# Optimization experiments

Measured on AMD Instinct MI355X. Metric: run time of the kernel, lower is better.

Reference implementation:

```python
import jax, jax.numpy as jnp
import numpy as np

NUM_HEADS = 12


def rotate_every_two(x):
    # interleaved rotation: (x0,x1,x2,x3,...) -> (-x1,x0,-x3,x2,...)
    x1 = x[..., ::2]
    x2 = x[..., 1::2]
    return jnp.stack((-x2, x1), axis=-1).reshape(x.shape)


def rope_cos_sin(seq_len, dim):
    # NOTE: faithfully replicates the source: freqs are concatenated
    # ([freqs, freqs]) even though rotation is interleaved.
    inv_freq = 1.0 / 10000.0 ** (jnp.arange(0, dim, 2, dtype=jnp.float32) / dim)
    t = jnp.arange(seq_len, dtype=jnp.float32)
    freqs = t[:, None] * inv_freq[None, :]          # [S, dim/2]
    emb = jnp.concatenate([freqs, freqs], axis=-1)  # [S, dim]
    return jnp.cos(emb)[None, None], jnp.sin(emb)[None, None]  # [1,1,S,dim]


def setup_inputs() -> dict:
    key = jax.random.key(0)
    kx, k1, k2, k3, k4 = jax.random.split(key, 5)
    B, S, D = 1, 4096, 768
    scale = 1.0 / np.sqrt(D)
    x = jax.random.normal(kx, (B, S, D), dtype=jnp.float32)
    W_qkv = jax.random.normal(k1, (D, 3 * D), dtype=jnp.float32) * scale
    b_qkv = jax.random.normal(k2, (3 * D,), dtype=jnp.float32) * 0.01
    W_out = jax.random.normal(k3, (D, D), dtype=jnp.float32) * scale
    b_out = jax.random.normal(k4, (D,), dtype=jnp.float32) * 0.01
    return {"x": x, "W_qkv": W_qkv, "b_qkv": b_qkv, "W_out": W_out, "b_out": b_out}


def reference(x, W_qkv, b_qkv, W_out, b_out):
    B, S, D = x.shape
    H = NUM_HEADS
    hd = D // H
    qkv = x @ W_qkv + b_qkv                         # [B,S,3D]
    qkv = qkv.reshape(B, S, 3, H, hd).transpose(2, 0, 3, 1, 4)  # [3,B,H,S,hd]
    q, k, v = qkv[0], qkv[1], qkv[2]
    cos, sin = rope_cos_sin(S, hd)
    q = q * cos + rotate_every_two(q) * sin
    k = k * cos + rotate_every_two(k) * sin
    scores = jnp.einsum('bhqd,bhkd->bhqk', q, k) / np.float32(np.sqrt(hd))
    probs = jax.nn.softmax(scores, axis=-1)
    ctx = jnp.einsum('bhqk,bhkd->bhqd', probs, v)   # [B,H,S,hd]
    ctx = ctx.transpose(0, 2, 1, 3).reshape(B, S, D)
    return ctx @ W_out + b_out
```

## Files before the change

### kernel.cpp

```cpp
#include <hip/hip_runtime.h>
#include <hip/hip_bf16.h>
#include <math.h>

#define S_LEN 4096
#define DMODEL 768
#define NH 12
#define HD 64

using f32x4 = __attribute__((ext_vector_type(4))) float;
using s16x8 = __attribute__((ext_vector_type(8))) short;

__device__ inline ushort f2bf(float f) {
  union { float f; uint32_t u; } v; v.f = f;
  uint32_t r = v.u + 0x7fffu + ((v.u >> 16) & 1u);
  return (ushort)(r >> 16);
}
__device__ __forceinline__ float fexp2(float x) {
  float r;
  asm("v_exp_f32 %0, %1" : "=v"(r) : "v"(x));
  return r;
}

__device__ __forceinline__ void gload16(const ushort* g, ushort* l) {
  __builtin_amdgcn_global_load_lds(
      (const __attribute__((address_space(1))) unsigned int*)g,
      (__attribute__((address_space(3))) unsigned int*)l, 16, 0, 0);
}

#define QSCL 0.18033688011112042f
#define L2_1E4_D32 0.4152410118655622f

__device__ void tsplit_dev(const float* __restrict__ W, ushort* __restrict__ Th,
                           int R, int C, int bx, int by,
                           int t, float (*tile)[33]) {
  const int tx = t & 31, ty = t >> 5;
  const int c0 = bx * 32, r0 = by * 32;
#pragma unroll
  for (int i = 0; i < 4; ++i)
    tile[ty + 8 * i][tx] = W[(size_t)(r0 + ty + 8 * i) * C + c0 + tx];
  __syncthreads();
#pragma unroll
  for (int i = 0; i < 4; ++i) {
    const float v = tile[tx][ty + 8 * i];
    const size_t off = (size_t)(c0 + ty + 8 * i) * R + r0 + tx;
    Th[off] = f2bf(v);
  }
}

__global__ __launch_bounds__(256) void k_prep(
    const float* __restrict__ x, const float* __restrict__ Wqkv,
    const float* __restrict__ Wout, float* __restrict__ ct,
    float* __restrict__ st, ushort* __restrict__ Wth,
    ushort* __restrict__ Woth, ushort* __restrict__ xh) {
  __shared__ float tile[32][33];
  const int b = blockIdx.x, t = threadIdx.x;
  if (b < 1024) {
    const int s = (b << 2) | (t >> 6), d = t & 63, j = d & 31;
    const float invf = fexp2(-L2_1E4_D32 * (float)j);
    const float af = (float)s * invf;
    ct[s * HD + d] = cosf(af);
    st[s * HD + d] = sinf(af);
  } else if (b < 2752) {
    const int bb = b - 1024;
    tsplit_dev(Wqkv, Wth, DMODEL, 3 * DMODEL, bb % 72, bb / 72, t, tile);
  } else if (b < 3328) {
    const int bb = b - 2752;
    tsplit_dev(Wout, Woth, DMODEL, DMODEL, bb % 24, bb / 24, t, tile);
  } else {
    const int i = (b - 3328) * 256 + t;
    const float4 v = ((const float4*)x)[i];
    ushort4 h;
    h.x = f2bf(v.x); h.y = f2bf(v.y); h.z = f2bf(v.z); h.w = f2bf(v.w);
    ((ushort4*)xh)[i] = h;
  }
}

template <int EPI, int BM, int TERMS>
__global__ __launch_bounds__(256) void k_gemm_split(
    const ushort* __restrict__ Ah, const ushort* __restrict__ Al,
    const ushort* __restrict__ Bh,
    const float* __restrict__ bias,
    const float* __restrict__ ct, const float* __restrict__ st,
    ushort* __restrict__ qh,
    ushort* __restrict__ kh, ushort* __restrict__ vt,
    float* __restrict__ out) {
  constexpr int MF = BM / 32;
  __shared__ __align__(16) ushort SS[(TERMS == 2 ? 2 : 1) * BM * 64 + 8192];
  constexpr int BOFF = (TERMS == 2 ? 2 : 1) * BM * 64;

  const int t = threadIdx.x;
  const int w = t >> 6, l = t & 63, g = l >> 4, lq = l & 15;
  const int wm = w >> 1, wn = w & 1;
  const int nbx = gridDim.x;
  int lin = blockIdx.y * nbx + blockIdx.x;
  const int cpx = (nbx * gridDim.y) >> 3;
  lin = (lin & 7) * cpx + (lin >> 3);
  const int m0 = (lin / nbx) * BM, n0 = (lin % nbx) * 128;

  f32x4 acc[MF][4];
#pragma unroll
  for (int i = 0; i < MF; ++i)
#pragma unroll
    for (int j = 0; j < 4; ++j) acc[i][j] = (f32x4){0.f, 0.f, 0.f, 0.f};

  const ushort* gsrc;
  ushort* lbase;
  int ninst;
  if (TERMS == 2) {
    if (w == 0)      { gsrc = Ah + (size_t)m0 * 768; lbase = SS;               ninst = BM / 16; }
    else if (w == 1) { gsrc = Ah + (size_t)(m0 + BM / 2) * 768; lbase = SS + BM * 32; ninst = BM / 16; }
    else if (w == 2) { gsrc = Al + (size_t)m0 * 768; lbase = SS + BM * 64;     ninst = BM / 8; }
    else             { gsrc = Bh + (size_t)n0 * 768; lbase = SS + BOFF;        ninst = 16; }
  } else {
    if (w == 0)      { gsrc = Ah + (size_t)m0 * 768; lbase = SS;               ninst = BM / 16; }
    else if (w == 1) { gsrc = Ah + (size_t)(m0 + BM / 2) * 768; lbase = SS + BM * 32; ninst = BM / 16; }
    else if (w == 2) { gsrc = Bh + (size_t)n0 * 768; lbase = SS + BOFF;        ninst = 8; }
    else             { gsrc = Bh + (size_t)(n0 + 64) * 768; lbase = SS + BOFF + 4096; ninst = 8; }
  }
  const int grow = l >> 3, gch = l & 7;
  gsrc += (size_t)grow * 768 + ((gch ^ grow) << 3);

  const ushort* rdA[2], * rdB[2];
#pragma unroll
  for (int kk = 0; kk < 2; ++kk) {
    rdA[kk] = SS + wm * (BM / 2) * 64 + lq * 64 + ((((kk << 2) | g) ^ (lq & 7)) << 3);
    rdB[kk] = SS + BOFF + wn * 4096 + lq * 64 + ((((kk << 2) | g) ^ (lq & 7)) << 3);
  }

  for (int kt = 0; kt < 768 / 64; ++kt) {
    __syncthreads();
#pragma unroll
    for (int i = 0; i < 16; ++i)
      if (i < ninst) gload16(gsrc + (size_t)i * (8 * 768) + kt * 64, lbase + i * 512);
    __syncthreads();
#pragma unroll
    for (int kk = 0; kk < 2; ++kk) {
      s16x8 ah[MF], al4[MF];
#pragma unroll
      for (int mf = 0; mf < MF; ++mf) {
        ah[mf] = *(const s16x8*)(rdA[kk] + mf * 1024);
        if (TERMS == 2) al4[mf] = *(const s16x8*)(rdA[kk] + mf * 1024 + BM * 64);
      }
      __builtin_amdgcn_s_setprio(1);
#pragma unroll
      for (int nf = 0; nf < 4; ++nf) {
        const s16x8 bhf = *(const s16x8*)(rdB[kk] + nf * 1024);
#pragma unroll
        for (int mf = 0; mf < MF; ++mf) {
          acc[mf][nf] = __builtin_amdgcn_mfma_f32_16x16x32_bf16(ah[mf], bhf, acc[mf][nf], 0, 0, 0);
          if (TERMS == 2)
            acc[mf][nf] = __builtin_amdgcn_mfma_f32_16x16x32_bf16(al4[mf], bhf, acc[mf][nf], 0, 0, 0);
        }
      }
      __builtin_amdgcn_s_setprio(0);
    }
  }

  if constexpr (EPI == 0) {
    const int cidx = n0 / DMODEL;
    if (cidx < 2) {
      ushort* dh = (cidx == 0) ? qh : kh;
      const float scl = (cidx == 0) ? QSCL : 1.0f;
#pragma unroll
      for (int nf = 0; nf < 4; ++nf) {
        const int n = n0 + wn * 64 + nf * 16 + lq;
        const int rem = n - cidx * DMODEL;
        const int hh = rem >> 6, d = rem & 63;
        const float sgn = (d & 1) ? 1.f : -1.f;
        const float bb = bias[n];
#pragma unroll
        for (int mf = 0; mf < MF; ++mf)
#pragma unroll
          for (int rg = 0; rg < 4; ++rg) {
            const int s = m0 + wm * (BM / 2) + mf * 16 + g * 4 + rg;
            const float v = acc[mf][nf][rg] + bb;
            const float vp = __shfl_xor(v, 1, 64);
            const float o = (v * ct[s * HD + d] + sgn * vp * st[s * HD + d]) * scl;
            const size_t off = (((size_t)hh * S_LEN + s) << 6) + d;
            dh[off] = f2bf(o);
          }
      }
    } else {
#pragma unroll
      for (int nf = 0; nf < 4; ++nf) {
        const int n = n0 + wn * 64 + nf * 16 + lq;
        const int rem = n - 2 * DMODEL;
        const int hh = rem >> 6, d = rem & 63;
        const float bb = bias[n];
#pragma unroll
        for (int mf = 0; mf < MF; ++mf) {
          union { ushort us[4]; ushort4 u4; } u;
#pragma unroll
          for (int rg = 0; rg < 4; ++rg) u.us[rg] = f2bf(acc[mf][nf][rg] + bb);
          const int sb = m0 + wm * (BM / 2) + mf * 16 + g * 4;
          const int sbp = (sb & ~31) | (g << 3) | ((mf & 1) << 2);
          *(ushort4*)(vt + ((size_t)hh * 64 + d) * S_LEN + sbp) = u.u4;
        }
      }
    }
  } else {
#pragma unroll
    for (int nf = 0; nf < 4; ++nf) {
      const int n = n0 + wn * 64 + nf * 16 + lq;
      const float bb = bias[n];
#pragma unroll
      for (int mf = 0; mf < MF; ++mf)
#pragma unroll
        for (int rg = 0; rg < 4; ++rg) {
          const int s = m0 + wm * (BM / 2) + mf * 16 + g * 4 + rg;
          out[(size_t)s * DMODEL + n] = acc[mf][nf][rg] + bb;
        }
    }
  }
}

__global__ __launch_bounds__(256) void k_attn_mfma(
    const ushort* __restrict__ qh,
    const ushort* __restrict__ kh, const ushort* __restrict__ vtp,
    ushort* __restrict__ cxh) {
  const int h = blockIdx.y;
  const int s0 = blockIdx.x << 6;
  const int t = threadIdx.x;
  const int w = t >> 6, l = t & 63, lq = l & 15, g = l >> 4;

  __shared__ __align__(16) ushort Ks0[2 * 4096];
  __shared__ __align__(16) ushort Vs0[2 * 4096];

  s16x8 qa0, qa1;
  {
    const size_t qoff = ((size_t)h * S_LEN + s0 + (w << 4) + lq) * 64 + (g << 3);
    qa0 = *(const s16x8*)(qh + qoff);
    qa1 = *(const s16x8*)(qh + qoff + 32);
  }
  s16x8 ones;
#pragma unroll
  for (int i = 0; i < 8; ++i) ones[i] = (short)0x3F80;

  f32x4 o[4];
#pragma unroll
  for (int m = 0; m < 4; ++m) o[m] = (f32x4){0.f, 0.f, 0.f, 0.f};
  f32x4 lacc = {0.f, 0.f, 0.f, 0.f};

  const int srow0 = (w << 4) + (l >> 3);
  const int sx = ((l & 7) ^ (l >> 3)) << 3;
  const ushort* gk = kh + ((size_t)h * S_LEN + srow0) * 64 + sx;
  const ushort* gv = vtp + (((size_t)h << 6) + srow0) * S_LEN + sx;
  ushort* ldK = Ks0 + srow0 * 64 + ((l & 7) << 3);
  ushort* ldV = Vs0 + srow0 * 64 + ((l & 7) << 3);

  auto stage = [&](const int kt, const int B) {
    const ushort* pk = gk + ((size_t)kt << 12);
    const ushort* pv = gv + (kt << 6);
    gload16(pk, ldK + B * 4096);
    gload16(pk + 512, ldK + B * 4096 + 512);
    gload16(pv, ldV + B * 4096);
    gload16(pv + (size_t)8 * S_LEN, ldV + B * 4096 + 512);
  };

  const int b0 = (lq << 6) | ((g ^ (lq & 7)) << 3);
  const int b1 = (lq << 6) | (((g + 4) ^ (lq & 7)) << 3);
  const ushort* kr0 = Ks0 + b0;
  const ushort* kr1 = Ks0 + b1;
  const ushort* vr0 = Vs0 + b0;
  const ushort* vr1 = Vs0 + b1;

  stage(0, 0);
  __syncthreads();

  auto body = [&](const int kt, const int CUR, const int NX, bool pref) {
    if (pref) stage(kt + 1, NX);

    f32x4 sc[4];
    __builtin_amdgcn_s_setprio(1);
#pragma unroll
    for (int n = 0; n < 4; ++n) {
      const s16x8 ka0 = *(const s16x8*)(kr0 + CUR * 4096 + (n << 10));
      const s16x8 ka1 = *(const s16x8*)(kr1 + CUR * 4096 + (n << 10));
      f32x4 a = {0.f, 0.f, 0.f, 0.f};
      a = __builtin_amdgcn_mfma_f32_16x16x32_bf16(ka0, qa0, a, 0, 0, 0);
      a = __builtin_amdgcn_mfma_f32_16x16x32_bf16(ka1, qa1, a, 0, 0, 0);
      sc[n] = a;
    }
    __builtin_amdgcn_s_setprio(0);

    float pr[4][4];
#pragma unroll
    for (int n = 0; n < 4; ++n)
#pragma unroll
      for (int rg = 0; rg < 4; ++rg) pr[n][rg] = fexp2(sc[n][rg]);

    uint32_t u[8];
#pragma unroll
    for (int n = 0; n < 4; ++n) {
      asm("v_cvt_pk_bf16_f32 %0, %1, %2"
          : "=v"(u[2 * n]) : "v"(pr[n][0]), "v"(pr[n][1]));
      asm("v_cvt_pk_bf16_f32 %0, %1, %2"
          : "=v"(u[2 * n + 1]) : "v"(pr[n][2]), "v"(pr[n][3]));
    }
    union { uint32_t uw[4]; s16x8 v; } p0, p1;
    p0.uw[0] = u[0]; p0.uw[1] = u[1]; p0.uw[2] = u[2]; p0.uw[3] = u[3];
    p1.uw[0] = u[4]; p1.uw[1] = u[5]; p1.uw[2] = u[6]; p1.uw[3] = u[7];

    __builtin_amdgcn_s_setprio(1);
    lacc = __builtin_amdgcn_mfma_f32_16x16x32_bf16(ones, p0.v, lacc, 0, 0, 0);
    lacc = __builtin_amdgcn_mfma_f32_16x16x32_bf16(ones, p1.v, lacc, 0, 0, 0);
#pragma unroll
    for (int m = 0; m < 4; ++m) {
      const s16x8 va0 = *(const s16x8*)(vr0 + CUR * 4096 + (m << 10));
      const s16x8 va1 = *(const s16x8*)(vr1 + CUR * 4096 + (m << 10));
      o[m] = __builtin_amdgcn_mfma_f32_16x16x32_bf16(va0, p0.v, o[m], 0, 0, 0);
      o[m] = __builtin_amdgcn_mfma_f32_16x16x32_bf16(va1, p1.v, o[m], 0, 0, 0);
    }
    __builtin_amdgcn_s_setprio(0);

    __syncthreads();
  };

  for (int p = 0; p < 32; ++p) {
    body(2 * p, 0, 1, true);
    body(2 * p + 1, 1, 0, p < 31);
  }

  const float inv = 1.0f / lacc[0];
  const size_t rowoff = (size_t)(s0 + (w << 4) + lq) * DMODEL + (h << 6) + (g << 2);
  ushort* hrow = cxh + rowoff;
#pragma unroll
  for (int m = 0; m < 4; ++m) {
    const float v0 = o[m][0] * inv, v1 = o[m][1] * inv;
    const float v2 = o[m][2] * inv, v3 = o[m][3] * inv;
    uint32_t h01, h23;
    asm("v_cvt_pk_bf16_f32 %0, %1, %2" : "=v"(h01) : "v"(v0), "v"(v1));
    asm("v_cvt_pk_bf16_f32 %0, %1, %2" : "=v"(h23) : "v"(v2), "v"(v3));
    uint2 hq;
    hq.x = h01; hq.y = h23;
    *(uint2*)(hrow + (m << 4)) = hq;
  }
}

extern "C" void kernel_launch(void* const* d_in, const int* in_sizes, int n_in,
                              void* d_out, int out_size, void* d_ws, size_t ws_size,
                              hipStream_t stream) {
  const float* x    = (const float*)d_in[0];
  const float* Wqkv = (const float*)d_in[1];
  const float* bqkv = (const float*)d_in[2];
  const float* Wout = (const float*)d_in[3];
  const float* bout = (const float*)d_in[4];
  float* out = (float*)d_out;

  const size_t NQ = (size_t)NH * S_LEN * HD;
  const size_t ND = (size_t)S_LEN * DMODEL;
  char* base = (char*)d_ws;
  ushort* qh = (ushort*)base;
  ushort* kh = qh + NQ;
  ushort* vt = kh + NQ;
  ushort* xh = vt + NQ;
  float* ct = (float*)(xh + ND);
  float* st = ct + (size_t)S_LEN * HD;
  ushort* Wth = (ushort*)(st + (size_t)S_LEN * HD);
  ushort* Woth = Wth + (size_t)3 * DMODEL * DMODEL;

  k_prep<<<dim3(6400), dim3(256), 0, stream>>>(
      x, Wqkv, Wout, ct, st, Wth, Woth, xh);
  k_gemm_split<0, 64, 1><<<dim3(3 * DMODEL / 128, S_LEN / 64), dim3(256), 0, stream>>>(
      xh, nullptr, Wth, bqkv, ct, st, qh, kh, vt, nullptr);
  k_attn_mfma<<<dim3(S_LEN / 64, NH), dim3(256), 0, stream>>>(
      qh, kh, vt, xh);
  k_gemm_split<1, 64, 1><<<dim3(DMODEL / 128, S_LEN / 64), dim3(256), 0, stream>>>(
      xh, nullptr, Woth, bout, nullptr, nullptr,
      nullptr, nullptr, nullptr, out);
}
```

Before: 123.2 us.

## Triple-buffer K/V tiles in attention with prefetch distance two

The attention kernel's K/V shared-memory staging grows from two buffers to three, so tile p+2 is loaded while tile p is computed. The per-iteration __syncthreads is replaced by an explicit s_waitcnt vmcnt(4) plus s_barrier, letting the newest prefetch stay in flight across the barrier. The aim is to hide more global-load latency behind the MFMA work. In exchange, LDS per block grows to 48KB, which may lower occupancy, and correctness now depends on the hand-written waitcnt counts.

Result: no change. 122.1 us (-0.9%).

```diff
diff --git a/kernel.cpp b/kernel.cpp
--- a/kernel.cpp
+++ b/kernel.cpp
@@ -223,8 +223,8 @@
   const int t = threadIdx.x;
   const int w = t >> 6, l = t & 63, lq = l & 15, g = l >> 4;
 
-  __shared__ __align__(16) ushort Ks0[2 * 4096];
-  __shared__ __align__(16) ushort Vs0[2 * 4096];
+  __shared__ __align__(16) ushort Ks0[3 * 4096];
+  __shared__ __align__(16) ushort Vs0[3 * 4096];
 
   s16x8 qa0, qa1;
   {
@@ -265,17 +265,21 @@
   const ushort* vr1 = Vs0 + b1;
 
   stage(0, 0);
-  __syncthreads();
-
-  auto body = [&](const int kt, const int CUR, const int NX, bool pref) {
-    if (pref) stage(kt + 1, NX);
+  stage(1, 1);
+  asm volatile("s_waitcnt vmcnt(4)" ::: "memory");
+  __builtin_amdgcn_sched_barrier(0);
+  __builtin_amdgcn_s_barrier();
+  __builtin_amdgcn_sched_barrier(0);
+
+  auto body = [&](const int p, const int B, const int NB, const bool pref) {
+    if (pref) stage(p + 2, NB);
 
     f32x4 sc[4];
     __builtin_amdgcn_s_setprio(1);
 #pragma unroll
     for (int n = 0; n < 4; ++n) {
-      const s16x8 ka0 = *(const s16x8*)(kr0 + CUR * 4096 + (n << 10));
-      const s16x8 ka1 = *(const s16x8*)(kr1 + CUR * 4096 + (n << 10));
+      const s16x8 ka0 = *(const s16x8*)(kr0 + B * 4096 + (n << 10));
+      const s16x8 ka1 = *(const s16x8*)(kr1 + B * 4096 + (n << 10));
       f32x4 a = {0.f, 0.f, 0.f, 0.f};
       a = __builtin_amdgcn_mfma_f32_16x16x32_bf16(ka0, qa0, a, 0, 0, 0);
       a = __builtin_amdgcn_mfma_f32_16x16x32_bf16(ka1, qa1, a, 0, 0, 0);
@@ -306,20 +310,27 @@
     lacc = __builtin_amdgcn_mfma_f32_16x16x32_bf16(ones, p1.v, lacc, 0, 0, 0);
 #pragma unroll
     for (int m = 0; m < 4; ++m) {
-      const s16x8 va0 = *(const s16x8*)(vr0 + CUR * 4096 + (m << 10));
-      const s16x8 va1 = *(const s16x8*)(vr1 + CUR * 4096 + (m << 10));
+      const s16x8 va0 = *(const s16x8*)(vr0 + B * 4096 + (m << 10));
+      const s16x8 va1 = *(const s16x8*)(vr1 + B * 4096 + (m << 10));
       o[m] = __builtin_amdgcn_mfma_f32_16x16x32_bf16(va0, p0.v, o[m], 0, 0, 0);
       o[m] = __builtin_amdgcn_mfma_f32_16x16x32_bf16(va1, p1.v, o[m], 0, 0, 0);
     }
     __builtin_amdgcn_s_setprio(0);
 
-    __syncthreads();
+    __builtin_amdgcn_sched_barrier(0);
+    if (pref) asm volatile("s_waitcnt vmcnt(4) lgkmcnt(0)" ::: "memory");
+    else      asm volatile("s_waitcnt vmcnt(0) lgkmcnt(0)" ::: "memory");
+    __builtin_amdgcn_sched_barrier(0);
+    __builtin_amdgcn_s_barrier();
+    __builtin_amdgcn_sched_barrier(0);
   };
 
-  for (int p = 0; p < 32; ++p) {
-    body(2 * p, 0, 1, true);
-    body(2 * p + 1, 1, 0, p < 31);
-  }
+  for (int c = 0; c < 21; ++c) {
+    body(3 * c + 0, 0, 2, true);
+    body(3 * c + 1, 1, 0, true);
+    body(3 * c + 2, 2, 1, c < 20);
+  }
+  body(63, 0, 2, false);
 
   const float inv = 1.0f / lacc[0];
   const size_t rowoff = (size_t)(s0 + (w << 4) + lq) * DMODEL + (h << 6) + (g << 2);
```

## Double-buffer LDS tiles in split GEMM to overlap global loads with MFMA

Applied to the files above, without the earlier changes.

Restructures the GEMM main loop to use two LDS buffers: the next k-tile is issued via global_load_lds into the alternate buffer while MFMAs consume the current one, with a single barrier per iteration. This aims to hide global-load latency and halve barrier count. It also drops the unused two-term (hi/lo) path. LDS usage doubles, which may lower occupancy.

After: 118.1 us. -4.1%, faster.

```diff
diff --git a/kernel.cpp b/kernel.cpp
--- a/kernel.cpp
+++ b/kernel.cpp
@@ -75,18 +75,17 @@
   }
 }
 
-template <int EPI, int BM, int TERMS>
+template <int EPI, int BM>
 __global__ __launch_bounds__(256) void k_gemm_split(
-    const ushort* __restrict__ Ah, const ushort* __restrict__ Al,
-    const ushort* __restrict__ Bh,
+    const ushort* __restrict__ Ah, const ushort* __restrict__ Bh,
     const float* __restrict__ bias,
     const float* __restrict__ ct, const float* __restrict__ st,
     ushort* __restrict__ qh,
     ushort* __restrict__ kh, ushort* __restrict__ vt,
     float* __restrict__ out) {
   constexpr int MF = BM / 32;
-  __shared__ __align__(16) ushort SS[(TERMS == 2 ? 2 : 1) * BM * 64 + 8192];
-  constexpr int BOFF = (TERMS == 2 ? 2 : 1) * BM * 64;
+  constexpr int SSH = BM * 64 + 8192;
+  __shared__ __align__(16) ushort SS[2 * SSH];
 
   const int t = threadIdx.x;
   const int w = t >> 6, l = t & 63, g = l >> 4, lq = l & 15;
@@ -106,54 +105,53 @@
   const ushort* gsrc;
   ushort* lbase;
   int ninst;
-  if (TERMS == 2) {
-    if (w == 0)      { gsrc = Ah + (size_t)m0 * 768; lbase = SS;               ninst = BM / 16; }
-    else if (w == 1) { gsrc = Ah + (size_t)(m0 + BM / 2) * 768; lbase = SS + BM * 32; ninst = BM / 16; }
-    else if (w == 2) { gsrc = Al + (size_t)m0 * 768; lbase = SS + BM * 64;     ninst = BM / 8; }
-    else             { gsrc = Bh + (size_t)n0 * 768; lbase = SS + BOFF;        ninst = 16; }
-  } else {
-    if (w == 0)      { gsrc = Ah + (size_t)m0 * 768; lbase = SS;               ninst = BM / 16; }
-    else if (w == 1) { gsrc = Ah + (size_t)(m0 + BM / 2) * 768; lbase = SS + BM * 32; ninst = BM / 16; }
-    else if (w == 2) { gsrc = Bh + (size_t)n0 * 768; lbase = SS + BOFF;        ninst = 8; }
-    else             { gsrc = Bh + (size_t)(n0 + 64) * 768; lbase = SS + BOFF + 4096; ninst = 8; }
-  }
+  if (w == 0)      { gsrc = Ah + (size_t)m0 * 768;            lbase = SS;                ninst = BM / 16; }
+  else if (w == 1) { gsrc = Ah + (size_t)(m0 + BM / 2) * 768; lbase = SS + BM * 32;      ninst = BM / 16; }
+  else if (w == 2) { gsrc = Bh + (size_t)n0 * 768;            lbase = SS + BM * 64;      ninst = 8; }
+  else             { gsrc = Bh + (size_t)(n0 + 64) * 768;     lbase = SS + BM * 64 + 4096; ninst = 8; }
   const int grow = l >> 3, gch = l & 7;
   gsrc += (size_t)grow * 768 + ((gch ^ grow) << 3);
 
+  auto gstage = [&](const int kt, const int B) {
+#pragma unroll
+    for (int i = 0; i < 16; ++i)
+      if (i < ninst)
+        gload16(gsrc + (size_t)i * (8 * 768) + kt * 64, lbase + B * SSH + i * 512);
+  };
+
   const ushort* rdA[2], * rdB[2];
 #pragma unroll
   for (int kk = 0; kk < 2; ++kk) {
     rdA[kk] = SS + wm * (BM / 2) * 64 + lq * 64 + ((((kk << 2) | g) ^ (lq & 7)) << 3);
-    rdB[kk] = SS + BOFF + wn * 4096 + lq * 64 + ((((kk << 2) | g) ^ (lq & 7)) << 3);
-  }
-
-  for (int kt = 0; kt < 768 / 64; ++kt) {
-    __syncthreads();
-#pragma unroll
-    for (int i = 0; i < 16; ++i)
-      if (i < ninst) gload16(gsrc + (size_t)i * (8 * 768) + kt * 64, lbase + i * 512);
-    __syncthreads();
+    rdB[kk] = SS + BM * 64 + wn * 4096 + lq * 64 + ((((kk << 2) | g) ^ (lq & 7)) << 3);
+  }
+
+  auto gbody = [&](const int kt, const int CUR, const int NX, const bool pref) {
+    if (pref) gstage(kt + 1, NX);
 #pragma unroll
     for (int kk = 0; kk < 2; ++kk) {
-      s16x8 ah[MF], al4[MF];
-#pragma unroll
-      for (int mf = 0; mf < MF; ++mf) {
-        ah[mf] = *(const s16x8*)(rdA[kk] + mf * 1024);
-        if (TERMS == 2) al4[mf] = *(const s16x8*)(rdA[kk] + mf * 1024 + BM * 64);
-      }
+      s16x8 ah[MF];
+#pragma unroll
+      for (int mf = 0; mf < MF; ++mf)
+        ah[mf] = *(const s16x8*)(rdA[kk] + CUR * SSH + mf * 1024);
       __builtin_amdgcn_s_setprio(1);
 #pragma unroll
       for (int nf = 0; nf < 4; ++nf) {
-        const s16x8 bhf = *(const s16x8*)(rdB[kk] + nf * 1024);
-#pragma unroll
-        for (int mf = 0; mf < MF; ++mf) {
+        const s16x8 bhf = *(const s16x8*)(rdB[kk] + CUR * SSH + nf * 1024);
+#pragma unroll
+        for (int mf = 0; mf < MF; ++mf)
           acc[mf][nf] = __builtin_amdgcn_mfma_f32_16x16x32_bf16(ah[mf], bhf, acc[mf][nf], 0, 0, 0);
-          if (TERMS == 2)
-            acc[mf][nf] = __builtin_amdgcn_mfma_f32_16x16x32_bf16(al4[mf], bhf, acc[mf][nf], 0, 0, 0);
-        }
       }
       __builtin_amdgcn_s_setprio(0);
     }
+    __syncthreads();
+  };
+
+  gstage(0, 0);
+  __syncthreads();
+  for (int p = 0; p < 6; ++p) {
+    gbody(2 * p, 0, 1, true);
+    gbody(2 * p + 1, 1, 0, p < 5);
   }
 
   if constexpr (EPI == 0) {
@@ -361,11 +359,11 @@
 
   k_prep<<<dim3(6400), dim3(256), 0, stream>>>(
       x, Wqkv, Wout, ct, st, Wth, Woth, xh);
-  k_gemm_split<0, 64, 1><<<dim3(3 * DMODEL / 128, S_LEN / 64), dim3(256), 0, stream>>>(
-      xh, nullptr, Wth, bqkv, ct, st, qh, kh, vt, nullptr);
+  k_gemm_split<0, 64><<<dim3(3 * DMODEL / 128, S_LEN / 64), dim3(256), 0, stream>>>(
+      xh, Wth, bqkv, ct, st, qh, kh, vt, nullptr);
   k_attn_mfma<<<dim3(S_LEN / 64, NH), dim3(256), 0, stream>>>(
       qh, kh, vt, xh);
-  k_gemm_split<1, 64, 1><<<dim3(DMODEL / 128, S_LEN / 64), dim3(256), 0, stream>>>(
-      xh, nullptr, Woth, bout, nullptr, nullptr,
+  k_gemm_split<1, 64><<<dim3(DMODEL / 128, S_LEN / 64), dim3(256), 0, stream>>>(
+      xh, Woth, bout, nullptr, nullptr,
       nullptr, nullptr, nullptr, out);
 }
```
